# Kernel optimization log

Measured on AMD Instinct MI355X. Metric: run time of the kernel, lower is better.

The kernel has to match this reference:

```python
import jax, jax.numpy as jnp
import numpy as np

N_QUBITS = 12
N_LAYERS = 6
BATCH = 512
DIM = 2 ** N_QUBITS


def _apply_1q(psi, G, wire):
    """Apply a single-qubit gate on `wire` (wire 0 = most significant).
    psi: [B, 2^n] complex. G: [2,2] (shared) or [B,2,2] (batched)."""
    B = psi.shape[0]
    left = 2 ** wire
    psi = psi.reshape(B, left, 2, -1)
    if G.ndim == 2:
        psi = jnp.einsum('ij,bxjy->bxiy', G, psi)
    else:
        psi = jnp.einsum('bij,bxjy->bxiy', G, psi)
    return psi.reshape(B, -1)


def _apply_cnot(psi, c, t):
    """CNOT with control c, target t on [B, 2^n] state."""
    B = psi.shape[0]
    ps = psi.reshape((B,) + (2,) * N_QUBITS)
    ca, ta = c + 1, t + 1
    c0 = jnp.take(ps, 0, axis=ca)
    c1 = jnp.take(ps, 1, axis=ca)
    flip_ax = ta if ta < ca else ta - 1
    c1 = jnp.flip(c1, axis=flip_ax)  # X on target within control=1 block
    ps = jnp.stack([c0, c1], axis=ca)
    return ps.reshape(B, -1)


def _circuit(x, weights):
    B = x.shape[0]
    psi = jnp.zeros((B, DIM), jnp.complex64).at[:, 0].set(1.0)

    # AngleEmbedding: RY(x_w) on each wire (batched gate matrices)
    h = 0.5 * x
    c, s = jnp.cos(h).astype(jnp.complex64), jnp.sin(h).astype(jnp.complex64)
    for w in range(N_QUBITS):
        G = jnp.stack([jnp.stack([c[:, w], -s[:, w]], -1),
                       jnp.stack([s[:, w], c[:, w]], -1)], -2)  # [B,2,2]
        psi = _apply_1q(psi, G, w)

    # StronglyEntanglingLayers: Rot(phi,theta,omega) per wire, then ring of CNOTs
    for l in range(N_LAYERS):
        phi, theta, omega = weights[l, :, 0], weights[l, :, 1], weights[l, :, 2]
        ct = jnp.cos(0.5 * theta).astype(jnp.complex64)
        st = jnp.sin(0.5 * theta).astype(jnp.complex64)
        ep = jnp.exp(-0.5j * (phi + omega).astype(jnp.complex64))
        em = jnp.exp(0.5j * (phi - omega).astype(jnp.complex64))
        # Rot = RZ(omega) RY(theta) RZ(phi)
        m00 = ep * ct
        m01 = -em * st
        m10 = jnp.conj(em) * st
        m11 = jnp.conj(ep) * ct
        for w in range(N_QUBITS):
            G = jnp.array([[m00[w], m01[w]], [m10[w], m11[w]]], jnp.complex64)
            psi = _apply_1q(psi, G, w)
        r = l % (N_QUBITS - 1) + 1
        for w in range(N_QUBITS):
            psi = _apply_cnot(psi, w, (w + r) % N_QUBITS)

    # <Z_w> for every wire
    probs = psi.real ** 2 + psi.imag ** 2  # [B, 2^n]
    exps = []
    for w in range(N_QUBITS):
        p = probs.reshape(B, 2 ** w, 2, -1)
        exps.append(p[:, :, 0, :].sum((1, 2)) - p[:, :, 1, :].sum((1, 2)))
    return jnp.stack(exps, -1)  # [B, n_qubits]


def setup_inputs() -> dict:
    key = jax.random.key(0)
    k1, k2, k3, k4 = jax.random.split(key, 4)
    x = jax.random.uniform(k1, (BATCH, N_QUBITS), jnp.float32, -np.pi, np.pi)
    weights = jax.random.uniform(k2, (N_LAYERS, N_QUBITS, 3), jnp.float32, 0.0, 2.0 * np.pi)
    W = jax.random.normal(k3, (1, N_QUBITS), jnp.float32) * 0.3
    b = jax.random.normal(k4, (1,), jnp.float32) * 0.01
    return {"x": x, "weights": weights, "W": W, "b": b}


def reference(x, weights, W, b):
    z = _circuit(x, weights)              # [B, n_qubits]
    y = z @ W.T + b                       # [B, 1]
    return y.squeeze(-1)                  # [B]
```

## Files before the change

### kernel.cpp

```cpp
#include <hip/hip_runtime.h>
#include <stdint.h>

#define NQ 12
#define DIM 4096
#define NLAYERS 6
#define TPB 256

typedef float v2f __attribute__((ext_vector_type(2)));

struct Pass_t {
    uint32_t WT[8];
    uint32_t WL[8];
    uint32_t RT[8];
    uint32_t RL[16];
};
struct Pass10_t {
    uint32_t WT[6];
    uint32_t WL[8];
    uint32_t RT[6];
    uint32_t RL[16];
};
struct CK_t {
    Pass10_t PA;
    Pass_t PB;
    Pass_t P1[NLAYERS];
    uint32_t frow[NQ];
};

constexpr uint32_t G2f(uint32_t k){ return ((k&15u)<<8) | (k&0xF0u) | ((k>>8)&15u); }
constexpr uint32_t G3f(uint32_t k){ return ((k&15u)<<4) | ((k>>4)&15u) | (k&0xF00u); }

constexpr uint32_t ech_reduce(const uint32_t* v, int n, uint32_t x){
    bool ch = true;
    while (ch) {
        ch = false;
        for (int i = 0; i < n; i++)
            if (v[i] && (x ^ v[i]) < x) { x ^= v[i]; ch = true; }
    }
    return x;
}

constexpr Pass_t build_pass(const uint32_t* Mc) {
    Pass_t P{};
    uint32_t rows[12]{};
    rows[0] = 8u;
    int nr = 1;
    uint32_t full[12]{}; int nf = 0; full[nf++] = 8u;
    uint32_t We[4]{};  int nw = 0;
    uint32_t Re[5]{};  int nre = 0;
    {
        uint32_t p0 = 0;
        for (int j = 0; j < 5; j++)
            p0 |= (uint32_t)(__builtin_popcount(8u & Mc[4 + j]) & 1) << j;
        uint32_t r = ech_reduce(Re, nre, p0);
        if (r) Re[nre++] = r;
    }
    for (int slot = 0; slot < 4; slot++) {
        uint32_t chosen = 0;
        for (int relax = 0; relax < 3 && !chosen; relax++) {
            for (uint32_t m = 1; m < 4096u && !chosen; m++) {
                if (m & 8u) continue;
                uint32_t wp = (m >> 4) & 15u;
                uint32_t wr = ech_reduce(We, nw, wp);
                if (relax < 2 && !wr) continue;
                uint32_t rp = 0;
                for (int j = 0; j < 5; j++)
                    rp |= (uint32_t)(__builtin_popcount(m & Mc[4 + j]) & 1) << j;
                uint32_t rr = ech_reduce(Re, nre, rp);
                if (relax < 1 && !rr) continue;
                uint32_t fr = ech_reduce(full, nf, m);
                if (!fr) continue;
                chosen = m; full[nf++] = fr;
                if (wr && nw < 4) We[nw++] = wr;
                if (rr && nre < 5) Re[nre++] = rr;
            }
        }
        rows[nr++] = chosen;
    }
    for (int slot = nr; slot < 12; slot++) {
        for (uint32_t m = 1; m < 4096u; m++) {
            if (m & 8u) continue;
            uint32_t fr = ech_reduce(full, nf, m);
            if (fr) { rows[slot] = m; full[nf++] = fr; break; }
        }
    }
    uint32_t col[12]{}, lmc[12]{};
    for (int j = 0; j < 12; j++) {
        uint32_t c = 0;
        for (int i = 0; i < 12; i++) c |= (uint32_t)((rows[i] >> j) & 1u) << i;
        col[j] = c;
    }
    for (int j = 0; j < 12; j++) {
        uint32_t a = 0, mc = Mc[j];
        for (int q = 0; q < 12; q++) if ((mc >> q) & 1u) a ^= col[q];
        lmc[j] = a;
    }
    for (int j = 0; j < 8; j++) { P.WT[j] = col[4 + j]; P.RT[j] = lmc[4 + j]; }
    for (int j = 0; j < 8; j++) {
        uint32_t a = 0;
        for (int q = 0; q < 3; q++) if ((j >> q) & 1) a ^= col[q];
        P.WL[j] = a;
    }
    for (int l = 0; l < 16; l++) {
        uint32_t a = 0;
        for (int q = 0; q < 4; q++) if ((l >> q) & 1) a ^= lmc[q];
        P.RL[l] = a;
    }
    return P;
}

constexpr Pass10_t build_pass10(const uint32_t* Mc) {
    Pass10_t P{};
    uint32_t rows[10]{};
    rows[0] = 8u;
    int nr = 1;
    uint32_t full[10]{}; int nf = 0; full[nf++] = 8u;
    uint32_t We[4]{};  int nw = 0;
    uint32_t Re[5]{};  int nre = 0;
    {
        uint32_t p0 = 0;
        for (int j = 0; j < 5; j++)
            p0 |= (uint32_t)(__builtin_popcount(8u & Mc[4 + j]) & 1) << j;
        uint32_t r = ech_reduce(Re, nre, p0);
        if (r) Re[nre++] = r;
    }
    for (int slot = 0; slot < 4; slot++) {
        uint32_t chosen = 0;
        for (int relax = 0; relax < 3 && !chosen; relax++) {
            for (uint32_t m = 1; m < 1024u && !chosen; m++) {
                if (m & 8u) continue;
                uint32_t wp = (m >> 4) & 15u;
                uint32_t wr = ech_reduce(We, nw, wp);
                if (relax < 2 && !wr) continue;
                uint32_t rp = 0;
                for (int j = 0; j < 5; j++)
                    rp |= (uint32_t)(__builtin_popcount(m & Mc[4 + j]) & 1) << j;
                uint32_t rr = ech_reduce(Re, nre, rp);
                if (relax < 1 && !rr) continue;
                uint32_t fr = ech_reduce(full, nf, m);
                if (!fr) continue;
                chosen = m; full[nf++] = fr;
                if (wr && nw < 4) We[nw++] = wr;
                if (rr && nre < 5) Re[nre++] = rr;
            }
        }
        rows[nr++] = chosen;
    }
    for (int slot = nr; slot < 10; slot++) {
        for (uint32_t m = 1; m < 1024u; m++) {
            if (m & 8u) continue;
            uint32_t fr = ech_reduce(full, nf, m);
            if (fr) { rows[slot] = m; full[nf++] = fr; break; }
        }
    }
    uint32_t col[10]{}, lmc[10]{};
    for (int j = 0; j < 10; j++) {
        uint32_t c = 0;
        for (int i = 0; i < 10; i++) c |= (uint32_t)((rows[i] >> j) & 1u) << i;
        col[j] = c;
    }
    for (int j = 0; j < 10; j++) {
        uint32_t a = 0, mc = Mc[j];
        for (int q = 0; q < 10; q++) if ((mc >> q) & 1u) a ^= col[q];
        lmc[j] = a;
    }
    for (int j = 0; j < 6; j++) { P.WT[j] = col[4 + j]; P.RT[j] = lmc[4 + j]; }
    for (int j = 0; j < 8; j++) {
        uint32_t a = 0;
        for (int q = 0; q < 3; q++) if ((j >> q) & 1) a ^= col[q];
        P.WL[j] = a;
    }
    for (int l = 0; l < 16; l++) {
        uint32_t a = 0;
        for (int q = 0; q < 4; q++) if ((l >> q) & 1) a ^= lmc[q];
        P.RL[l] = a;
    }
    return P;
}

constexpr CK_t build_ck() {
    CK_t ck{};
    uint32_t Acols[NLAYERS][NQ]{}, Aicol5[NQ]{};
    for (int l = 0; l < NLAYERS; l++) {
        int r = l % (NQ - 1) + 1;
        for (int q = 0; q < NQ; q++) {
            uint32_t v = 1u << q;
            for (int w = NQ - 1; w >= 0; w--) {
                int pc = NQ - 1 - w, pt = NQ - 1 - ((w + r) % NQ);
                v ^= ((v >> pc) & 1u) << pt;
            }
            Acols[l][q] = v;
            if (l == NLAYERS - 1) {
                uint32_t u = 1u << q;
                for (int w = 0; w < NQ; w++) {
                    int pc = NQ - 1 - w, pt = NQ - 1 - ((w + r) % NQ);
                    u ^= ((u >> pc) & 1u) << pt;
                }
                Aicol5[q] = u;
            }
        }
    }
    uint32_t Mc10[10]{};
    for (int j = 0; j < 10; j++) Mc10[j] = G3f(1u << j);
    ck.PA = build_pass10(Mc10);
    uint32_t Mc[12]{};
    for (int j = 0; j < 12; j++) Mc[j] = G2f(1u << j);
    ck.PB = build_pass(Mc);
    for (int l = 1; l < NLAYERS; l++) {
        for (int j = 0; j < 12; j++) Mc[j] = G2f(G3f(Acols[l - 1][j]));
        ck.P1[l] = build_pass(Mc);
    }
    uint32_t Mcol[NQ]{};
    for (int j = 0; j < NQ; j++) {
        uint32_t pj = G3f(G2f(1u << j));
        uint32_t M = 0;
        for (int m = 0; m < NQ; m++) if ((pj >> m) & 1u) M ^= Aicol5[m];
        Mcol[j] = M;
    }
    for (int p = 0; p < NQ; p++) {
        uint32_t s = 0;
        for (int j = 0; j < NQ; j++) s |= ((Mcol[j] >> p) & 1u) << j;
        ck.frow[p] = s;
    }
    return ck;
}
constexpr CK_t CK = build_ck();

template<int Q>
__device__ __forceinline__ void gate_q(v2f (&PRE)[8], v2f (&PIM)[8], float4 m) {
    v2f bx = {m.x, m.x}, by = {m.y, m.y}, bz = {m.z, m.z}, bw = {m.w, m.w};
    #pragma unroll
    for (int j = 0; j < 8; j++) {
        if (j & (1 << Q)) continue;
        int j2 = j | (1 << Q);
        v2f re0 = PRE[j], im0 = PIM[j], re1 = PRE[j2], im1 = PIM[j2];
        PRE[j]  = __builtin_elementwise_fma(bx, re0,
                  __builtin_elementwise_fma(by, -im0,
                  __builtin_elementwise_fma(bz, re1, -bw * im1)));
        PIM[j]  = __builtin_elementwise_fma(bx, im0,
                  __builtin_elementwise_fma(by, re0,
                  __builtin_elementwise_fma(bz, im1, bw * re1)));
        PRE[j2] = __builtin_elementwise_fma(bx, re1,
                  __builtin_elementwise_fma(by, im1,
                  __builtin_elementwise_fma(bz, -re0, -bw * im0)));
        PIM[j2] = __builtin_elementwise_fma(bx, im1,
                  __builtin_elementwise_fma(by, -re1,
                  __builtin_elementwise_fma(bz, -im0, bw * re0)));
    }
}

__device__ __forceinline__ void pack_gate(v2f (&PRE)[8], v2f (&PIM)[8], float4 m) {
    v2f d1 = {-m.y, m.y}, d2 = {m.z, -m.z};
    #pragma unroll
    for (int j = 0; j < 8; j++) {
        v2f RE = PRE[j], IM = PIM[j];
        v2f sR = {RE.y, RE.x}, sI = {IM.y, IM.x};
        PRE[j] = m.x * RE + d1 * IM + d2 * sR - m.w * sI;
        PIM[j] = m.x * IM - d1 * RE + d2 * sI + m.w * sR;
    }
}

__device__ __forceinline__ void pa_pass(v2f (&PRE)[8], v2f (&PIM)[8],
                                        float* buf, uint32_t wb, uint32_t rb) {
    constexpr Pass10_t P = CK.PA;
    v2f* bre = (v2f*)buf;
    v2f* bim = (v2f*)(buf + DIM);
    #pragma unroll
    for (int j = 0; j < 8; j++) {
        uint32_t s = (wb ^ P.WL[j]) >> 1;
        bre[s] = PRE[j]; bim[s] = PIM[j];
    }
    __asm__ volatile("s_waitcnt lgkmcnt(0)" ::: "memory");
    #pragma unroll
    for (int j = 0; j < 8; j++) {
        uint32_t s0 = rb ^ P.RL[j], s1 = rb ^ P.RL[j | 8];
        v2f re, im;
        re.x = buf[s0];       re.y = buf[s1];
        im.x = buf[DIM + s0]; im.y = buf[DIM + s1];
        PRE[j] = re; PIM[j] = im;
    }
}

__device__ __forceinline__ void pb_pass(v2f (&PRE)[8], v2f (&PIM)[8],
                                        float* buf, uint32_t wb, uint32_t rb) {
    constexpr Pass_t P = CK.PB;
    v2f* bre = (v2f*)buf;
    v2f* bim = (v2f*)(buf + DIM);
    __syncthreads();
    #pragma unroll
    for (int j = 0; j < 8; j++) {
        uint32_t s = (wb ^ P.WL[j]) >> 1;
        bre[s] = PRE[j]; bim[s] = PIM[j];
    }
    __syncthreads();
    #pragma unroll
    for (int j = 0; j < 8; j++) {
        uint32_t s0 = rb ^ P.RL[j], s1 = rb ^ P.RL[j | 8];
        v2f re, im;
        re.x = buf[s0];       re.y = buf[s1];
        im.x = buf[DIM + s0]; im.y = buf[DIM + s1];
        PRE[j] = re; PIM[j] = im;
    }
}

__device__ __forceinline__ void rebase_pass(v2f (&PRE)[8], v2f (&PIM)[8],
                                            float* buf, int tid, int l) {
    const Pass_t& P = CK.P1[l];
    uint32_t wb = 0, rb = 0;
    #pragma unroll
    for (int j = 0; j < 8; j++) {
        uint32_t sel = (uint32_t)(-(int)((tid >> j) & 1));
        wb ^= sel & P.WT[j];
        rb ^= sel & P.RT[j];
    }
    v2f* bre = (v2f*)buf;
    v2f* bim = (v2f*)(buf + DIM);
    #pragma unroll
    for (int j = 0; j < 8; j++) {
        uint32_t s = (wb ^ P.WL[j]) >> 1;
        bre[s] = PRE[j]; bim[s] = PIM[j];
    }
    __syncthreads();
    #pragma unroll
    for (int j = 0; j < 8; j++) {
        uint32_t s0 = rb ^ P.RL[j], s1 = rb ^ P.RL[j | 8];
        v2f re, im;
        re.x = buf[s0];       re.y = buf[s1];
        im.x = buf[DIM + s0]; im.y = buf[DIM + s1];
        PRE[j] = re; PIM[j] = im;
    }
}

__global__ __launch_bounds__(TPB) void qsim_kernel(
    const float* __restrict__ x,
    const float* __restrict__ weights,
    const float* __restrict__ Wp,
    const float* __restrict__ bptr,
    float* __restrict__ out)
{
    __shared__ float  lds[2 * 2 * DIM];
    __shared__ float4 smat[NLAYERS * NQ];
    __shared__ float  scs[NQ], sss[NQ];
    __shared__ float  red[4];

    const int tid = threadIdx.x;
    const int b   = blockIdx.x;

    if (tid < NQ) {
        float s_, c_;
        sincosf(0.5f * x[b * NQ + tid], &s_, &c_);
        scs[tid] = c_; sss[tid] = s_;
    }
    if (tid < NLAYERS * NQ) {
        float phi   = weights[tid * 3 + 0];
        float theta = weights[tid * 3 + 1];
        float omega = weights[tid * 3 + 2];
        float st, ct; sincosf(0.5f * theta, &st, &ct);
        float sp, cp; sincosf(0.5f * (phi + omega), &sp, &cp);
        float sm, cm; sincosf(0.5f * (phi - omega), &sm, &cm);
        smat[tid] = make_float4(cp * ct, -sp * ct, -cm * st, -sm * st);
    }
    __syncthreads();

    float base = 1.0f;
    #pragma unroll
    for (int j = 0; j < 8; j++) {
        int w = 7 - j;
        base *= ((tid >> j) & 1) ? sss[w] : scs[w];
    }
    v2f PRE[8], PIM[8];
    float c8 = scs[8], s8 = sss[8];
    #pragma unroll
    for (int j = 0; j < 8; j++) {
        float a = base;
        #pragma unroll
        for (int p = 0; p < 3; p++) {
            int w = NQ - 1 - p;
            a *= ((j >> p) & 1) ? sss[w] : scs[w];
        }
        PRE[j].x = a * c8;  PRE[j].y = a * s8;
        PIM[j].x = 0.0f;    PIM[j].y = 0.0f;
    }

    uint32_t pawb = 0, parb = 0, pbwb = 0, pbrb = 0;
    #pragma unroll
    for (int j = 0; j < 6; j++) {
        uint32_t sel = (uint32_t)(-(int)((tid >> j) & 1));
        pawb ^= sel & CK.PA.WT[j]; parb ^= sel & CK.PA.RT[j];
    }
    #pragma unroll
    for (int j = 0; j < 8; j++) {
        uint32_t sel = (uint32_t)(-(int)((tid >> j) & 1));
        pbwb ^= sel & CK.PB.WT[j]; pbrb ^= sel & CK.PB.RT[j];
    }
    {
        uint32_t wvb = (uint32_t)(tid & 0xC0) << 4;
        pawb |= wvb; parb |= wvb;
    }

    float* bufA = lds;
    float* bufB = lds + 2 * DIM;

    #pragma clang loop unroll(disable)
    for (int l = 0; l < NLAYERS; l++) {
        if (l > 0) rebase_pass(PRE, PIM, bufB, tid, l);
        const int sb = l * NQ;
        gate_q<0>(PRE, PIM, smat[sb + 11]);
        gate_q<1>(PRE, PIM, smat[sb + 10]);
        gate_q<2>(PRE, PIM, smat[sb + 9]);
        pack_gate(PRE, PIM, smat[sb + 8]);
        pa_pass(PRE, PIM, bufA, pawb, parb);
        gate_q<0>(PRE, PIM, smat[sb + 7]);
        gate_q<1>(PRE, PIM, smat[sb + 6]);
        gate_q<2>(PRE, PIM, smat[sb + 5]);
        pack_gate(PRE, PIM, smat[sb + 4]);
        pb_pass(PRE, PIM, bufA, pbwb, pbrb);
        gate_q<0>(PRE, PIM, smat[sb + 3]);
        gate_q<1>(PRE, PIM, smat[sb + 2]);
        gate_q<2>(PRE, PIM, smat[sb + 1]);
        pack_gate(PRE, PIM, smat[sb + 0]);
    }

    const float bv = bptr[0];
    float wbT[NQ];
    #pragma unroll
    for (int p = 0; p < NQ; p++) {
        uint32_t row = CK.frow[p];
        int tp = __popc(tid & (int)(row >> 4)) & 1;
        float Wv = Wp[NQ - 1 - p];
        wbT[p] = tp ? -Wv : Wv;
    }
    v2f acc2 = {0.0f, 0.0f};
    #pragma unroll
    for (int j = 0; j < 8; j++) {
        float cx = bv, cy = bv;
        #pragma unroll
        for (int p = 0; p < NQ; p++) {
            uint32_t row = CK.frow[p];
            float s = (__popc(j & (int)(row & 7u)) & 1) ? -wbT[p] : wbT[p];
            cx += s;
            cy += (row & 8u) ? -s : s;
        }
        v2f c = {cx, cy};
        acc2 += (PRE[j] * PRE[j] + PIM[j] * PIM[j]) * c;
    }
    float acc = acc2.x + acc2.y;
    #pragma unroll
    for (int off = 32; off > 0; off >>= 1)
        acc += __shfl_down(acc, off, 64);
    if ((tid & 63) == 0) red[tid >> 6] = acc;
    __syncthreads();
    if (tid == 0) out[b] = red[0] + red[1] + red[2] + red[3];
}

extern "C" void kernel_launch(void* const* d_in, const int* in_sizes, int n_in,
                              void* d_out, int out_size, void* d_ws, size_t ws_size,
                              hipStream_t stream) {
    const float* x       = (const float*)d_in[0];
    const float* weights = (const float*)d_in[1];
    const float* W       = (const float*)d_in[2];
    const float* bptr    = (const float*)d_in[3];
    qsim_kernel<<<512, TPB, 0, stream>>>(x, weights, W, bptr, (float*)d_out);
}
```

Measured before the change: 91.34 us.

## Use 512 threads per batch element with 8 amplitudes per thread

Doubles the threads per block from 256 to 512, so each thread holds 8 amplitudes (4 packed pairs) instead of 16. The layer is split into three LDS exchange passes (two wave-local, one block-wide) with 3 qubits handled in registers between passes, and the GF(2) permutation tables are rebuilt for the new bit layout. The goal is more parallelism and lower register pressure per thread, at the cost of an extra LDS exchange per layer and more threads taking part in each sync.

```diff
diff --git a/kernel.cpp b/kernel.cpp
--- a/kernel.cpp
+++ b/kernel.cpp
@@ -4,31 +4,33 @@
 #define NQ 12
 #define DIM 4096
 #define NLAYERS 6
-#define TPB 256
+#define TPB 512
 
 typedef float v2f __attribute__((ext_vector_type(2)));
 
 struct Pass_t {
-    uint32_t WT[8];
-    uint32_t WL[8];
-    uint32_t RT[8];
-    uint32_t RL[16];
+    uint32_t WT[9];
+    uint32_t WL[4];
+    uint32_t RT[9];
+    uint32_t RL[8];
 };
-struct Pass10_t {
+struct Pass9_t {
     uint32_t WT[6];
-    uint32_t WL[8];
+    uint32_t WL[4];
     uint32_t RT[6];
-    uint32_t RL[16];
+    uint32_t RL[8];
 };
 struct CK_t {
-    Pass10_t PA;
+    Pass9_t PA1;
+    Pass9_t PA2;
     Pass_t PB;
     Pass_t P1[NLAYERS];
     uint32_t frow[NQ];
 };
 
-constexpr uint32_t G2f(uint32_t k){ return ((k&15u)<<8) | (k&0xF0u) | ((k>>8)&15u); }
-constexpr uint32_t G3f(uint32_t k){ return ((k&15u)<<4) | ((k>>4)&15u) | (k&0xF00u); }
+constexpr uint32_t S1f(uint32_t k){ return (k & 0xFC0u) | ((k & 7u) << 3) | ((k >> 3) & 7u); }
+constexpr uint32_t S2f(uint32_t k){ return (k & 0xE38u) | ((k & 7u) << 6) | ((k >> 6) & 7u); }
+constexpr uint32_t S3f(uint32_t k){ return (k & 0x1F8u) | ((k & 7u) << 9) | ((k >> 9) & 7u); }
 
 constexpr uint32_t ech_reduce(const uint32_t* v, int n, uint32_t x){
     bool ch = true;
@@ -43,15 +45,15 @@
 constexpr Pass_t build_pass(const uint32_t* Mc) {
     Pass_t P{};
     uint32_t rows[12]{};
-    rows[0] = 8u;
+    rows[0] = 4u;
     int nr = 1;
-    uint32_t full[12]{}; int nf = 0; full[nf++] = 8u;
+    uint32_t full[12]{}; int nf = 0; full[nf++] = 4u;
     uint32_t We[4]{};  int nw = 0;
     uint32_t Re[5]{};  int nre = 0;
     {
         uint32_t p0 = 0;
         for (int j = 0; j < 5; j++)
-            p0 |= (uint32_t)(__builtin_popcount(8u & Mc[4 + j]) & 1) << j;
+            p0 |= (uint32_t)(__builtin_popcount(4u & Mc[3 + j]) & 1) << j;
         uint32_t r = ech_reduce(Re, nre, p0);
         if (r) Re[nre++] = r;
     }
@@ -59,13 +61,13 @@
         uint32_t chosen = 0;
         for (int relax = 0; relax < 3 && !chosen; relax++) {
             for (uint32_t m = 1; m < 4096u && !chosen; m++) {
-                if (m & 8u) continue;
-                uint32_t wp = (m >> 4) & 15u;
+                if (m & 4u) continue;
+                uint32_t wp = (m >> 3) & 15u;
                 uint32_t wr = ech_reduce(We, nw, wp);
                 if (relax < 2 && !wr) continue;
                 uint32_t rp = 0;
                 for (int j = 0; j < 5; j++)
-                    rp |= (uint32_t)(__builtin_popcount(m & Mc[4 + j]) & 1) << j;
+                    rp |= (uint32_t)(__builtin_popcount(m & Mc[3 + j]) & 1) << j;
                 uint32_t rr = ech_reduce(Re, nre, rp);
                 if (relax < 1 && !rr) continue;
                 uint32_t fr = ech_reduce(full, nf, m);
@@ -79,7 +81,7 @@
     }
     for (int slot = nr; slot < 12; slot++) {
         for (uint32_t m = 1; m < 4096u; m++) {
-            if (m & 8u) continue;
+            if (m & 4u) continue;
             uint32_t fr = ech_reduce(full, nf, m);
             if (fr) { rows[slot] = m; full[nf++] = fr; break; }
         }
@@ -95,46 +97,46 @@
         for (int q = 0; q < 12; q++) if ((mc >> q) & 1u) a ^= col[q];
         lmc[j] = a;
     }
-    for (int j = 0; j < 8; j++) { P.WT[j] = col[4 + j]; P.RT[j] = lmc[4 + j]; }
-    for (int j = 0; j < 8; j++) {
+    for (int j = 0; j < 9; j++) { P.WT[j] = col[3 + j]; P.RT[j] = lmc[3 + j]; }
+    for (int j = 0; j < 4; j++) {
         uint32_t a = 0;
-        for (int q = 0; q < 3; q++) if ((j >> q) & 1) a ^= col[q];
+        for (int q = 0; q < 2; q++) if ((j >> q) & 1) a ^= col[q];
         P.WL[j] = a;
     }
-    for (int l = 0; l < 16; l++) {
+    for (int l = 0; l < 8; l++) {
         uint32_t a = 0;
-        for (int q = 0; q < 4; q++) if ((l >> q) & 1) a ^= lmc[q];
+        for (int q = 0; q < 3; q++) if ((l >> q) & 1) a ^= lmc[q];
         P.RL[l] = a;
     }
     return P;
 }
 
-constexpr Pass10_t build_pass10(const uint32_t* Mc) {
-    Pass10_t P{};
-    uint32_t rows[10]{};
-    rows[0] = 8u;
+constexpr Pass9_t build_pass9(const uint32_t* Mc) {
+    Pass9_t P{};
+    uint32_t rows[9]{};
+    rows[0] = 4u;
     int nr = 1;
-    uint32_t full[10]{}; int nf = 0; full[nf++] = 8u;
+    uint32_t full[9]{}; int nf = 0; full[nf++] = 4u;
     uint32_t We[4]{};  int nw = 0;
     uint32_t Re[5]{};  int nre = 0;
     {
         uint32_t p0 = 0;
         for (int j = 0; j < 5; j++)
-            p0 |= (uint32_t)(__builtin_popcount(8u & Mc[4 + j]) & 1) << j;
+            p0 |= (uint32_t)(__builtin_popcount(4u & Mc[3 + j]) & 1) << j;
         uint32_t r = ech_reduce(Re, nre, p0);
         if (r) Re[nre++] = r;
     }
     for (int slot = 0; slot < 4; slot++) {
         uint32_t chosen = 0;
         for (int relax = 0; relax < 3 && !chosen; relax++) {
-            for (uint32_t m = 1; m < 1024u && !chosen; m++) {
-                if (m & 8u) continue;
-                uint32_t wp = (m >> 4) & 15u;
+            for (uint32_t m = 1; m < 512u && !chosen; m++) {
+                if (m & 4u) continue;
+                uint32_t wp = (m >> 3) & 15u;
                 uint32_t wr = ech_reduce(We, nw, wp);
                 if (relax < 2 && !wr) continue;
                 uint32_t rp = 0;
                 for (int j = 0; j < 5; j++)
-                    rp |= (uint32_t)(__builtin_popcount(m & Mc[4 + j]) & 1) << j;
+                    rp |= (uint32_t)(__builtin_popcount(m & Mc[3 + j]) & 1) << j;
                 uint32_t rr = ech_reduce(Re, nre, rp);
                 if (relax < 1 && !rr) continue;
                 uint32_t fr = ech_reduce(full, nf, m);
@@ -146,33 +148,33 @@
         }
         rows[nr++] = chosen;
     }
-    for (int slot = nr; slot < 10; slot++) {
-        for (uint32_t m = 1; m < 1024u; m++) {
-            if (m & 8u) continue;
+    for (int slot = nr; slot < 9; slot++) {
+        for (uint32_t m = 1; m < 512u; m++) {
+            if (m & 4u) continue;
             uint32_t fr = ech_reduce(full, nf, m);
             if (fr) { rows[slot] = m; full[nf++] = fr; break; }
         }
     }
-    uint32_t col[10]{}, lmc[10]{};
-    for (int j = 0; j < 10; j++) {
+    uint32_t col[9]{}, lmc[9]{};
+    for (int j = 0; j < 9; j++) {
         uint32_t c = 0;
-        for (int i = 0; i < 10; i++) c |= (uint32_t)((rows[i] >> j) & 1u) << i;
+        for (int i = 0; i < 9; i++) c |= (uint32_t)((rows[i] >> j) & 1u) << i;
         col[j] = c;
     }
-    for (int j = 0; j < 10; j++) {
+    for (int j = 0; j < 9; j++) {
         uint32_t a = 0, mc = Mc[j];
-        for (int q = 0; q < 10; q++) if ((mc >> q) & 1u) a ^= col[q];
+        for (int q = 0; q < 9; q++) if ((mc >> q) & 1u) a ^= col[q];
         lmc[j] = a;
     }
-    for (int j = 0; j < 6; j++) { P.WT[j] = col[4 + j]; P.RT[j] = lmc[4 + j]; }
-    for (int j = 0; j < 8; j++) {
+    for (int j = 0; j < 6; j++) { P.WT[j] = col[3 + j]; P.RT[j] = lmc[3 + j]; }
+    for (int j = 0; j < 4; j++) {
         uint32_t a = 0;
-        for (int q = 0; q < 3; q++) if ((j >> q) & 1) a ^= col[q];
+        for (int q = 0; q < 2; q++) if ((j >> q) & 1) a ^= col[q];
         P.WL[j] = a;
     }
-    for (int l = 0; l < 16; l++) {
+    for (int l = 0; l < 8; l++) {
         uint32_t a = 0;
-        for (int q = 0; q < 4; q++) if ((l >> q) & 1) a ^= lmc[q];
+        for (int q = 0; q < 3; q++) if ((l >> q) & 1) a ^= lmc[q];
         P.RL[l] = a;
     }
     return P;
@@ -200,19 +202,21 @@
             }
         }
     }
-    uint32_t Mc10[10]{};
-    for (int j = 0; j < 10; j++) Mc10[j] = G3f(1u << j);
-    ck.PA = build_pass10(Mc10);
+    uint32_t Mc9[9]{};
+    for (int j = 0; j < 9; j++) Mc9[j] = S1f(1u << j);
+    ck.PA1 = build_pass9(Mc9);
+    for (int j = 0; j < 9; j++) Mc9[j] = S2f(1u << j);
+    ck.PA2 = build_pass9(Mc9);
     uint32_t Mc[12]{};
-    for (int j = 0; j < 12; j++) Mc[j] = G2f(1u << j);
+    for (int j = 0; j < 12; j++) Mc[j] = S3f(1u << j);
     ck.PB = build_pass(Mc);
     for (int l = 1; l < NLAYERS; l++) {
-        for (int j = 0; j < 12; j++) Mc[j] = G2f(G3f(Acols[l - 1][j]));
+        for (int j = 0; j < 12; j++) Mc[j] = S3f(S2f(S1f(Acols[l - 1][j])));
         ck.P1[l] = build_pass(Mc);
     }
     uint32_t Mcol[NQ]{};
     for (int j = 0; j < NQ; j++) {
-        uint32_t pj = G3f(G2f(1u << j));
+        uint32_t pj = S1f(S2f(S3f(1u << j)));
         uint32_t M = 0;
         for (int m = 0; m < NQ; m++) if ((pj >> m) & 1u) M ^= Aicol5[m];
         Mcol[j] = M;
@@ -227,10 +231,10 @@
 constexpr CK_t CK = build_ck();
 
 template<int Q>
-__device__ __forceinline__ void gate_q(v2f (&PRE)[8], v2f (&PIM)[8], float4 m) {
+__device__ __forceinline__ void gate_q(v2f (&PRE)[4], v2f (&PIM)[4], float4 m) {
     v2f bx = {m.x, m.x}, by = {m.y, m.y}, bz = {m.z, m.z}, bw = {m.w, m.w};
     #pragma unroll
-    for (int j = 0; j < 8; j++) {
+    for (int j = 0; j < 4; j++) {
         if (j & (1 << Q)) continue;
         int j2 = j | (1 << Q);
         v2f re0 = PRE[j], im0 = PIM[j], re1 = PRE[j2], im1 = PIM[j2];
@@ -249,10 +253,10 @@
     }
 }
 
-__device__ __forceinline__ void pack_gate(v2f (&PRE)[8], v2f (&PIM)[8], float4 m) {
+__device__ __forceinline__ void pack_gate(v2f (&PRE)[4], v2f (&PIM)[4], float4 m) {
     v2f d1 = {-m.y, m.y}, d2 = {m.z, -m.z};
     #pragma unroll
-    for (int j = 0; j < 8; j++) {
+    for (int j = 0; j < 4; j++) {
         v2f RE = PRE[j], IM = PIM[j];
         v2f sR = {RE.y, RE.x}, sI = {IM.y, IM.x};
         PRE[j] = m.x * RE + d1 * IM + d2 * sR - m.w * sI;
@@ -260,20 +264,22 @@
     }
 }
 
-__device__ __forceinline__ void pa_pass(v2f (&PRE)[8], v2f (&PIM)[8],
+template<int IDX>
+__device__ __forceinline__ void wl_pass(v2f (&PRE)[4], v2f (&PIM)[4],
                                         float* buf, uint32_t wb, uint32_t rb) {
-    constexpr Pass10_t P = CK.PA;
+    constexpr Pass9_t P = (IDX == 0) ? CK.PA1 : CK.PA2;
     v2f* bre = (v2f*)buf;
     v2f* bim = (v2f*)(buf + DIM);
-    #pragma unroll
-    for (int j = 0; j < 8; j++) {
+    __asm__ volatile("s_waitcnt lgkmcnt(0)" ::: "memory");
+    #pragma unroll
+    for (int j = 0; j < 4; j++) {
         uint32_t s = (wb ^ P.WL[j]) >> 1;
         bre[s] = PRE[j]; bim[s] = PIM[j];
     }
     __asm__ volatile("s_waitcnt lgkmcnt(0)" ::: "memory");
     #pragma unroll
-    for (int j = 0; j < 8; j++) {
-        uint32_t s0 = rb ^ P.RL[j], s1 = rb ^ P.RL[j | 8];
+    for (int j = 0; j < 4; j++) {
+        uint32_t s0 = rb ^ P.RL[j], s1 = rb ^ P.RL[j | 4];
         v2f re, im;
         re.x = buf[s0];       re.y = buf[s1];
         im.x = buf[DIM + s0]; im.y = buf[DIM + s1];
@@ -281,21 +287,21 @@
     }
 }
 
-__device__ __forceinline__ void pb_pass(v2f (&PRE)[8], v2f (&PIM)[8],
+__device__ __forceinline__ void p3_pass(v2f (&PRE)[4], v2f (&PIM)[4],
                                         float* buf, uint32_t wb, uint32_t rb) {
     constexpr Pass_t P = CK.PB;
     v2f* bre = (v2f*)buf;
     v2f* bim = (v2f*)(buf + DIM);
     __syncthreads();
     #pragma unroll
-    for (int j = 0; j < 8; j++) {
+    for (int j = 0; j < 4; j++) {
         uint32_t s = (wb ^ P.WL[j]) >> 1;
         bre[s] = PRE[j]; bim[s] = PIM[j];
     }
     __syncthreads();
     #pragma unroll
-    for (int j = 0; j < 8; j++) {
-        uint32_t s0 = rb ^ P.RL[j], s1 = rb ^ P.RL[j | 8];
+    for (int j = 0; j < 4; j++) {
+        uint32_t s0 = rb ^ P.RL[j], s1 = rb ^ P.RL[j | 4];
         v2f re, im;
         re.x = buf[s0];       re.y = buf[s1];
         im.x = buf[DIM + s0]; im.y = buf[DIM + s1];
@@ -303,12 +309,12 @@
     }
 }
 
-__device__ __forceinline__ void rebase_pass(v2f (&PRE)[8], v2f (&PIM)[8],
+__device__ __forceinline__ void rebase_pass(v2f (&PRE)[4], v2f (&PIM)[4],
                                             float* buf, int tid, int l) {
     const Pass_t& P = CK.P1[l];
     uint32_t wb = 0, rb = 0;
     #pragma unroll
-    for (int j = 0; j < 8; j++) {
+    for (int j = 0; j < 9; j++) {
         uint32_t sel = (uint32_t)(-(int)((tid >> j) & 1));
         wb ^= sel & P.WT[j];
         rb ^= sel & P.RT[j];
@@ -316,14 +322,14 @@
     v2f* bre = (v2f*)buf;
     v2f* bim = (v2f*)(buf + DIM);
     #pragma unroll
-    for (int j = 0; j < 8; j++) {
+    for (int j = 0; j < 4; j++) {
         uint32_t s = (wb ^ P.WL[j]) >> 1;
         bre[s] = PRE[j]; bim[s] = PIM[j];
     }
     __syncthreads();
     #pragma unroll
-    for (int j = 0; j < 8; j++) {
-        uint32_t s0 = rb ^ P.RL[j], s1 = rb ^ P.RL[j | 8];
+    for (int j = 0; j < 4; j++) {
+        uint32_t s0 = rb ^ P.RL[j], s1 = rb ^ P.RL[j | 4];
         v2f re, im;
         re.x = buf[s0];       re.y = buf[s1];
         im.x = buf[DIM + s0]; im.y = buf[DIM + s1];
@@ -331,7 +337,7 @@
     }
 }
 
-__global__ __launch_bounds__(TPB) void qsim_kernel(
+__global__ __launch_bounds__(TPB, 4) void qsim_kernel(
     const float* __restrict__ x,
     const float* __restrict__ weights,
     const float* __restrict__ Wp,
@@ -341,7 +347,7 @@
     __shared__ float  lds[2 * 2 * DIM];
     __shared__ float4 smat[NLAYERS * NQ];
     __shared__ float  scs[NQ], sss[NQ];
-    __shared__ float  red[4];
+    __shared__ float  red[8];
 
     const int tid = threadIdx.x;
     const int b   = blockIdx.x;
@@ -364,38 +370,39 @@
 
     float base = 1.0f;
     #pragma unroll
-    for (int j = 0; j < 8; j++) {
-        int w = 7 - j;
-        base *= ((tid >> j) & 1) ? sss[w] : scs[w];
-    }
-    v2f PRE[8], PIM[8];
-    float c8 = scs[8], s8 = sss[8];
-    #pragma unroll
-    for (int j = 0; j < 8; j++) {
+    for (int t = 0; t < 9; t++) {
+        int w = 8 - t;
+        base *= ((tid >> t) & 1) ? sss[w] : scs[w];
+    }
+    v2f PRE[4], PIM[4];
+    float c9 = scs[9], s9 = sss[9];
+    #pragma unroll
+    for (int j = 0; j < 4; j++) {
         float a = base;
         #pragma unroll
-        for (int p = 0; p < 3; p++) {
+        for (int p = 0; p < 2; p++) {
             int w = NQ - 1 - p;
             a *= ((j >> p) & 1) ? sss[w] : scs[w];
         }
-        PRE[j].x = a * c8;  PRE[j].y = a * s8;
+        PRE[j].x = a * c9;  PRE[j].y = a * s9;
         PIM[j].x = 0.0f;    PIM[j].y = 0.0f;
     }
 
-    uint32_t pawb = 0, parb = 0, pbwb = 0, pbrb = 0;
+    uint32_t p1wb = 0, p1rb = 0, p2wb = 0, p2rb = 0, p3wb = 0, p3rb = 0;
     #pragma unroll
     for (int j = 0; j < 6; j++) {
         uint32_t sel = (uint32_t)(-(int)((tid >> j) & 1));
-        pawb ^= sel & CK.PA.WT[j]; parb ^= sel & CK.PA.RT[j];
-    }
-    #pragma unroll
-    for (int j = 0; j < 8; j++) {
+        p1wb ^= sel & CK.PA1.WT[j]; p1rb ^= sel & CK.PA1.RT[j];
+        p2wb ^= sel & CK.PA2.WT[j]; p2rb ^= sel & CK.PA2.RT[j];
+    }
+    #pragma unroll
+    for (int j = 0; j < 9; j++) {
         uint32_t sel = (uint32_t)(-(int)((tid >> j) & 1));
-        pbwb ^= sel & CK.PB.WT[j]; pbrb ^= sel & CK.PB.RT[j];
+        p3wb ^= sel & CK.PB.WT[j]; p3rb ^= sel & CK.PB.RT[j];
     }
     {
-        uint32_t wvb = (uint32_t)(tid & 0xC0) << 4;
-        pawb |= wvb; parb |= wvb;
+        uint32_t wvb = (uint32_t)(tid & 0x1C0) << 3;
+        p1wb |= wvb; p1rb |= wvb; p2wb |= wvb; p2rb |= wvb;
     }
 
     float* bufA = lds;
@@ -407,17 +414,18 @@
         const int sb = l * NQ;
         gate_q<0>(PRE, PIM, smat[sb + 11]);
         gate_q<1>(PRE, PIM, smat[sb + 10]);
-        gate_q<2>(PRE, PIM, smat[sb + 9]);
-        pack_gate(PRE, PIM, smat[sb + 8]);
-        pa_pass(PRE, PIM, bufA, pawb, parb);
-        gate_q<0>(PRE, PIM, smat[sb + 7]);
-        gate_q<1>(PRE, PIM, smat[sb + 6]);
-        gate_q<2>(PRE, PIM, smat[sb + 5]);
-        pack_gate(PRE, PIM, smat[sb + 4]);
-        pb_pass(PRE, PIM, bufA, pbwb, pbrb);
-        gate_q<0>(PRE, PIM, smat[sb + 3]);
-        gate_q<1>(PRE, PIM, smat[sb + 2]);
-        gate_q<2>(PRE, PIM, smat[sb + 1]);
+        pack_gate(PRE, PIM, smat[sb + 9]);
+        wl_pass<0>(PRE, PIM, bufA, p1wb, p1rb);
+        gate_q<0>(PRE, PIM, smat[sb + 8]);
+        gate_q<1>(PRE, PIM, smat[sb + 7]);
+        pack_gate(PRE, PIM, smat[sb + 6]);
+        wl_pass<1>(PRE, PIM, bufA, p2wb, p2rb);
+        gate_q<0>(PRE, PIM, smat[sb + 5]);
+        gate_q<1>(PRE, PIM, smat[sb + 4]);
+        pack_gate(PRE, PIM, smat[sb + 3]);
+        p3_pass(PRE, PIM, bufA, p3wb, p3rb);
+        gate_q<0>(PRE, PIM, smat[sb + 2]);
+        gate_q<1>(PRE, PIM, smat[sb + 1]);
         pack_gate(PRE, PIM, smat[sb + 0]);
     }
 
@@ -426,20 +434,20 @@
     #pragma unroll
     for (int p = 0; p < NQ; p++) {
         uint32_t row = CK.frow[p];
-        int tp = __popc(tid & (int)(row >> 4)) & 1;
+        int tp = __popc(tid & (int)(row >> 3)) & 1;
         float Wv = Wp[NQ - 1 - p];
         wbT[p] = tp ? -Wv : Wv;
     }
     v2f acc2 = {0.0f, 0.0f};
     #pragma unroll
-    for (int j = 0; j < 8; j++) {
+    for (int j = 0; j < 4; j++) {
         float cx = bv, cy = bv;
         #pragma unroll
         for (int p = 0; p < NQ; p++) {
             uint32_t row = CK.frow[p];
-            float s = (__popc(j & (int)(row & 7u)) & 1) ? -wbT[p] : wbT[p];
+            float s = (__popc(j & (int)(row & 3u)) & 1) ? -wbT[p] : wbT[p];
             cx += s;
-            cy += (row & 8u) ? -s : s;
+            cy += (row & 4u) ? -s : s;
         }
         v2f c = {cx, cy};
         acc2 += (PRE[j] * PRE[j] + PIM[j] * PIM[j]) * c;
@@ -450,7 +458,12 @@
         acc += __shfl_down(acc, off, 64);
     if ((tid & 63) == 0) red[tid >> 6] = acc;
     __syncthreads();
-    if (tid == 0) out[b] = red[0] + red[1] + red[2] + red[3];
+    if (tid == 0) {
+        float r = 0.0f;
+        #pragma unroll
+        for (int wv = 0; wv < 8; wv++) r += red[wv];
+        out[b] = r;
+    }
 }
 
 extern "C" void kernel_launch(void* const* d_in, const int* in_sizes, int n_in,
```

Result: no change. 90.72 us (-0.7%).

## Process two batch samples per block and interleave their gate and LDS passes

Applied to the files above, without the earlier changes.

Each block now simulates two batch elements, keeping two register-resident state vectors and alternating their compute and LDS exchange phases so one sample's gate arithmetic can hide the other's shared-memory traffic and barriers. The grid halves to 256 blocks, LDS grows to 24 KB per block, and launch bounds are set to one block's worth of waves per SIMD to allow more registers. The trade is fewer blocks than the device's compute units, which can leave CUs idle, plus much higher register pressure from the doubled state.

```diff
diff --git a/kernel.cpp b/kernel.cpp
--- a/kernel.cpp
+++ b/kernel.cpp
@@ -260,8 +260,18 @@
     }
 }
 
-__device__ __forceinline__ void pa_pass(v2f (&PRE)[8], v2f (&PIM)[8],
-                                        float* buf, uint32_t wb, uint32_t rb) {
+__device__ __forceinline__ void winq(v2f (&PRE)[8], v2f (&PIM)[8], const float4* p) {
+    gate_q<0>(PRE, PIM, p[3]);
+    gate_q<1>(PRE, PIM, p[2]);
+    gate_q<2>(PRE, PIM, p[1]);
+}
+__device__ __forceinline__ void win(v2f (&PRE)[8], v2f (&PIM)[8], const float4* p) {
+    winq(PRE, PIM, p);
+    pack_gate(PRE, PIM, p[0]);
+}
+
+__device__ __forceinline__ void pa_w(const v2f (&PRE)[8], const v2f (&PIM)[8],
+                                     float* buf, uint32_t wb) {
     constexpr Pass10_t P = CK.PA;
     v2f* bre = (v2f*)buf;
     v2f* bim = (v2f*)(buf + DIM);
@@ -270,6 +280,10 @@
         uint32_t s = (wb ^ P.WL[j]) >> 1;
         bre[s] = PRE[j]; bim[s] = PIM[j];
     }
+}
+__device__ __forceinline__ void pa_r(v2f (&PRE)[8], v2f (&PIM)[8],
+                                     const float* buf, uint32_t rb) {
+    constexpr Pass10_t P = CK.PA;
     __asm__ volatile("s_waitcnt lgkmcnt(0)" ::: "memory");
     #pragma unroll
     for (int j = 0; j < 8; j++) {
@@ -281,21 +295,21 @@
     }
 }
 
-__device__ __forceinline__ void pb_pass(v2f (&PRE)[8], v2f (&PIM)[8],
-                                        float* buf, uint32_t wb, uint32_t rb) {
-    constexpr Pass_t P = CK.PB;
+__device__ __forceinline__ void cross_w(const v2f (&PRE)[8], const v2f (&PIM)[8],
+                                        float* buf, uint32_t wb, const uint32_t* WL) {
     v2f* bre = (v2f*)buf;
     v2f* bim = (v2f*)(buf + DIM);
-    __syncthreads();
-    #pragma unroll
-    for (int j = 0; j < 8; j++) {
-        uint32_t s = (wb ^ P.WL[j]) >> 1;
+    #pragma unroll
+    for (int j = 0; j < 8; j++) {
+        uint32_t s = (wb ^ WL[j]) >> 1;
         bre[s] = PRE[j]; bim[s] = PIM[j];
     }
-    __syncthreads();
-    #pragma unroll
-    for (int j = 0; j < 8; j++) {
-        uint32_t s0 = rb ^ P.RL[j], s1 = rb ^ P.RL[j | 8];
+}
+__device__ __forceinline__ void cross_r(v2f (&PRE)[8], v2f (&PIM)[8],
+                                        const float* buf, uint32_t rb, const uint32_t* RL) {
+    #pragma unroll
+    for (int j = 0; j < 8; j++) {
+        uint32_t s0 = rb ^ RL[j], s1 = rb ^ RL[j | 8];
         v2f re, im;
         re.x = buf[s0];       re.y = buf[s1];
         im.x = buf[DIM + s0]; im.y = buf[DIM + s1];
@@ -303,53 +317,54 @@
     }
 }
 
-__device__ __forceinline__ void rebase_pass(v2f (&PRE)[8], v2f (&PIM)[8],
-                                            float* buf, int tid, int l) {
-    const Pass_t& P = CK.P1[l];
-    uint32_t wb = 0, rb = 0;
-    #pragma unroll
-    for (int j = 0; j < 8; j++) {
-        uint32_t sel = (uint32_t)(-(int)((tid >> j) & 1));
-        wb ^= sel & P.WT[j];
-        rb ^= sel & P.RT[j];
-    }
-    v2f* bre = (v2f*)buf;
-    v2f* bim = (v2f*)(buf + DIM);
-    #pragma unroll
-    for (int j = 0; j < 8; j++) {
-        uint32_t s = (wb ^ P.WL[j]) >> 1;
-        bre[s] = PRE[j]; bim[s] = PIM[j];
-    }
-    __syncthreads();
-    #pragma unroll
-    for (int j = 0; j < 8; j++) {
-        uint32_t s0 = rb ^ P.RL[j], s1 = rb ^ P.RL[j | 8];
-        v2f re, im;
-        re.x = buf[s0];       re.y = buf[s1];
-        im.x = buf[DIM + s0]; im.y = buf[DIM + s1];
-        PRE[j] = re; PIM[j] = im;
-    }
-}
-
-__global__ __launch_bounds__(TPB) void qsim_kernel(
+__device__ __forceinline__ void init_state(v2f (&PRE)[8], v2f (&PIM)[8],
+                                           const float* scs, const float* sss, int tid) {
+    float base = 1.0f;
+    #pragma unroll
+    for (int j = 0; j < 8; j++) {
+        int w = 7 - j;
+        base *= ((tid >> j) & 1) ? sss[w] : scs[w];
+    }
+    float c8 = scs[8], s8 = sss[8];
+    #pragma unroll
+    for (int j = 0; j < 8; j++) {
+        float a = base;
+        #pragma unroll
+        for (int p = 0; p < 3; p++) {
+            int w = NQ - 1 - p;
+            a *= ((j >> p) & 1) ? sss[w] : scs[w];
+        }
+        PRE[j].x = a * c8;  PRE[j].y = a * s8;
+        PIM[j].x = 0.0f;    PIM[j].y = 0.0f;
+    }
+}
+
+__global__ __launch_bounds__(TPB, 1) void qsim_kernel(
     const float* __restrict__ x,
     const float* __restrict__ weights,
     const float* __restrict__ Wp,
     const float* __restrict__ bptr,
     float* __restrict__ out)
 {
-    __shared__ float  lds[2 * 2 * DIM];
+    __shared__ float  lds[6 * DIM];
     __shared__ float4 smat[NLAYERS * NQ];
-    __shared__ float  scs[NQ], sss[NQ];
-    __shared__ float  red[4];
+    __shared__ float  scsA[NQ], sssA[NQ], scsB[NQ], sssB[NQ];
+    __shared__ float  red[8];
 
     const int tid = threadIdx.x;
     const int b   = blockIdx.x;
+    const int bA  = 2 * b, bB = 2 * b + 1;
 
     if (tid < NQ) {
         float s_, c_;
-        sincosf(0.5f * x[b * NQ + tid], &s_, &c_);
-        scs[tid] = c_; sss[tid] = s_;
+        sincosf(0.5f * x[bA * NQ + tid], &s_, &c_);
+        scsA[tid] = c_; sssA[tid] = s_;
+    }
+    if (tid >= 64 && tid < 64 + NQ) {
+        int q = tid - 64;
+        float s_, c_;
+        sincosf(0.5f * x[bB * NQ + q], &s_, &c_);
+        scsB[q] = c_; sssB[q] = s_;
     }
     if (tid < NLAYERS * NQ) {
         float phi   = weights[tid * 3 + 0];
@@ -362,25 +377,9 @@
     }
     __syncthreads();
 
-    float base = 1.0f;
-    #pragma unroll
-    for (int j = 0; j < 8; j++) {
-        int w = 7 - j;
-        base *= ((tid >> j) & 1) ? sss[w] : scs[w];
-    }
-    v2f PRE[8], PIM[8];
-    float c8 = scs[8], s8 = sss[8];
-    #pragma unroll
-    for (int j = 0; j < 8; j++) {
-        float a = base;
-        #pragma unroll
-        for (int p = 0; p < 3; p++) {
-            int w = NQ - 1 - p;
-            a *= ((j >> p) & 1) ? sss[w] : scs[w];
-        }
-        PRE[j].x = a * c8;  PRE[j].y = a * s8;
-        PIM[j].x = 0.0f;    PIM[j].y = 0.0f;
-    }
+    v2f PRA[8], PIA[8], PRB[8], PIB[8];
+    init_state(PRA, PIA, scsA, sssA, tid);
+    init_state(PRB, PIB, scsB, sssB, tid);
 
     uint32_t pawb = 0, parb = 0, pbwb = 0, pbrb = 0;
     #pragma unroll
@@ -398,28 +397,67 @@
         pawb |= wvb; parb |= wvb;
     }
 
-    float* bufA = lds;
-    float* bufB = lds + 2 * DIM;
+    float* pabuf = lds;
+    float* bufXA = lds + 2 * DIM;
+    float* bufXB = lds + 4 * DIM;
+
+    {
+        win(PRA, PIA, &smat[8]);
+        pa_w(PRA, PIA, pabuf, pawb);
+        win(PRB, PIB, &smat[8]);
+        pa_r(PRA, PIA, pabuf, parb);
+        pa_w(PRB, PIB, pabuf, pawb);
+        win(PRA, PIA, &smat[4]);
+        pa_r(PRB, PIB, pabuf, parb);
+        cross_w(PRA, PIA, bufXA, pbwb, CK.PB.WL);
+        win(PRB, PIB, &smat[4]);
+        cross_w(PRB, PIB, bufXB, pbwb, CK.PB.WL);
+        __syncthreads();
+        cross_r(PRA, PIA, bufXA, pbrb, CK.PB.RL);
+        cross_r(PRB, PIB, bufXB, pbrb, CK.PB.RL);
+        winq(PRA, PIA, &smat[0]);
+        winq(PRB, PIB, &smat[0]);
+        __syncthreads();
+        pack_gate(PRA, PIA, smat[0]);
+    }
 
     #pragma clang loop unroll(disable)
-    for (int l = 0; l < NLAYERS; l++) {
-        if (l > 0) rebase_pass(PRE, PIM, bufB, tid, l);
-        const int sb = l * NQ;
-        gate_q<0>(PRE, PIM, smat[sb + 11]);
-        gate_q<1>(PRE, PIM, smat[sb + 10]);
-        gate_q<2>(PRE, PIM, smat[sb + 9]);
-        pack_gate(PRE, PIM, smat[sb + 8]);
-        pa_pass(PRE, PIM, bufA, pawb, parb);
-        gate_q<0>(PRE, PIM, smat[sb + 7]);
-        gate_q<1>(PRE, PIM, smat[sb + 6]);
-        gate_q<2>(PRE, PIM, smat[sb + 5]);
-        pack_gate(PRE, PIM, smat[sb + 4]);
-        pb_pass(PRE, PIM, bufA, pbwb, pbrb);
-        gate_q<0>(PRE, PIM, smat[sb + 3]);
-        gate_q<1>(PRE, PIM, smat[sb + 2]);
-        gate_q<2>(PRE, PIM, smat[sb + 1]);
-        pack_gate(PRE, PIM, smat[sb + 0]);
-    }
+    for (int l = 1; l < NLAYERS; l++) {
+        const Pass_t& P = CK.P1[l];
+        uint32_t rwb = 0, rrb = 0;
+        #pragma unroll
+        for (int j = 0; j < 8; j++) {
+            uint32_t sel = (uint32_t)(-(int)((tid >> j) & 1));
+            rwb ^= sel & P.WT[j];
+            rrb ^= sel & P.RT[j];
+        }
+        const int sb = l * NQ, sp = (l - 1) * NQ;
+
+        cross_w(PRA, PIA, bufXA, rwb, P.WL);
+        pack_gate(PRB, PIB, smat[sp + 0]);
+        cross_w(PRB, PIB, bufXB, rwb, P.WL);
+        __syncthreads();
+        cross_r(PRA, PIA, bufXA, rrb, P.RL);
+        cross_r(PRB, PIB, bufXB, rrb, P.RL);
+        win(PRA, PIA, &smat[sb + 8]);
+        pa_w(PRA, PIA, pabuf, pawb);
+        win(PRB, PIB, &smat[sb + 8]);
+        pa_r(PRA, PIA, pabuf, parb);
+        pa_w(PRB, PIB, pabuf, pawb);
+        win(PRA, PIA, &smat[sb + 4]);
+        pa_r(PRB, PIB, pabuf, parb);
+        cross_w(PRA, PIA, bufXA, pbwb, CK.PB.WL);
+        win(PRB, PIB, &smat[sb + 4]);
+        cross_w(PRB, PIB, bufXB, pbwb, CK.PB.WL);
+        __syncthreads();
+        cross_r(PRA, PIA, bufXA, pbrb, CK.PB.RL);
+        cross_r(PRB, PIB, bufXB, pbrb, CK.PB.RL);
+        winq(PRA, PIA, &smat[sb + 0]);
+        winq(PRB, PIB, &smat[sb + 0]);
+        __syncthreads();
+        pack_gate(PRA, PIA, smat[sb + 0]);
+    }
+    pack_gate(PRB, PIB, smat[(NLAYERS - 1) * NQ + 0]);
 
     const float bv = bptr[0];
     float wbT[NQ];
@@ -430,7 +468,7 @@
         float Wv = Wp[NQ - 1 - p];
         wbT[p] = tp ? -Wv : Wv;
     }
-    v2f acc2 = {0.0f, 0.0f};
+    v2f accA2 = {0.0f, 0.0f}, accB2 = {0.0f, 0.0f};
     #pragma unroll
     for (int j = 0; j < 8; j++) {
         float cx = bv, cy = bv;
@@ -442,15 +480,23 @@
             cy += (row & 8u) ? -s : s;
         }
         v2f c = {cx, cy};
-        acc2 += (PRE[j] * PRE[j] + PIM[j] * PIM[j]) * c;
-    }
-    float acc = acc2.x + acc2.y;
-    #pragma unroll
-    for (int off = 32; off > 0; off >>= 1)
-        acc += __shfl_down(acc, off, 64);
-    if ((tid & 63) == 0) red[tid >> 6] = acc;
+        accA2 += (PRA[j] * PRA[j] + PIA[j] * PIA[j]) * c;
+        accB2 += (PRB[j] * PRB[j] + PIB[j] * PIB[j]) * c;
+    }
+    float accA = accA2.x + accA2.y;
+    float accB = accB2.x + accB2.y;
+    #pragma unroll
+    for (int off = 32; off > 0; off >>= 1) {
+        accA += __shfl_down(accA, off, 64);
+        accB += __shfl_down(accB, off, 64);
+    }
+    if ((tid & 63) == 0) {
+        red[tid >> 6]       = accA;
+        red[(tid >> 6) + 4] = accB;
+    }
     __syncthreads();
-    if (tid == 0) out[b] = red[0] + red[1] + red[2] + red[3];
+    if (tid == 0) out[bA] = red[0] + red[1] + red[2] + red[3];
+    if (tid == 1) out[bB] = red[4] + red[5] + red[6] + red[7];
 }
 
 extern "C" void kernel_launch(void* const* d_in, const int* in_sizes, int n_in,
@@ -460,5 +506,5 @@
     const float* weights = (const float*)d_in[1];
     const float* W       = (const float*)d_in[2];
     const float* bptr    = (const float*)d_in[3];
-    qsim_kernel<<<512, TPB, 0, stream>>>(x, weights, W, bptr, (float*)d_out);
-}
+    qsim_kernel<<<256, TPB, 0, stream>>>(x, weights, W, bptr, (float*)d_out);
+}
```

Result: slower. 98.80 us (+8.2%).
